# Performance work log

Measured on AMD Instinct MI355X. Metric: run time of the kernel, lower is better.

## Reference

```python
import jax, jax.numpy as jnp
import numpy as np

BN_EPS = 1e-3  # keras BatchNormalization default epsilon


def conv1x1(x, w):
    # x: [N,C,H,W], w: [O,C] (1x1 conv, no bias)
    return jnp.einsum('nchw,oc->nohw', x, w)


def bn(x, gamma, beta, mean, var):
    # inference-mode batchnorm over channel axis 1
    scale = gamma / jnp.sqrt(var + BN_EPS)
    shift = beta - mean * scale
    return x * scale[None, :, None, None] + shift[None, :, None, None]


def fourier_unit(x, w, gamma, beta, mean, var):
    # x: [N,C,H,W] NCHW. 1D rfft over W (matches tf.signal.rfft), normalized by sqrt(W).
    N, C, H, W = x.shape
    norm = jnp.sqrt(jnp.float32(W))
    f = jnp.fft.rfft(x / norm, axis=-1)          # [N,C,H,Wf] complex64, Wf=W//2+1
    Wf = f.shape[-1]
    # interleave re/im per channel: [N,C,2,H,Wf] -> [N,2C,H,Wf]
    ff = jnp.stack([jnp.real(f), jnp.imag(f)], axis=2).reshape(N, 2 * C, H, Wf)
    y = jax.nn.relu(bn(conv1x1(ff, w), gamma, beta, mean, var))  # [N,2C,H,Wf]
    Co = y.shape[1] // 2
    y = y.reshape(N, Co, 2, H, Wf)
    c = jax.lax.complex(y[:, :, 0], y[:, :, 1])
    return jnp.fft.irfft(c, n=W, axis=-1) * norm  # [N,Co,H,W]


def setup_inputs() -> dict:
    key = jax.random.key(0)
    ks = jax.random.split(key, 20)
    N, H, W, Cin = 8, 128, 128, 256
    fmaps = 256
    half = fmaps // 2  # 128

    def nrm(k, shape, s=0.05):
        return jax.random.normal(k, shape, dtype=jnp.float32) * s

    def bn_params(k, c):
        k1, k2, k3, k4 = jax.random.split(k, 4)
        gamma = jax.random.uniform(k1, (c,), dtype=jnp.float32) + 0.5
        beta = nrm(k2, (c,), 0.1)
        mean = nrm(k3, (c,), 0.1)
        var = jax.random.uniform(k4, (c,), dtype=jnp.float32) + 0.5
        return gamma, beta, mean, var

    x = jax.random.normal(ks[0], (N, H, W, Cin), dtype=jnp.float32)
    w1 = nrm(ks[1], (half, Cin))
    g1, b1, m1, v1 = bn_params(ks[2], half)
    fu_w = nrm(ks[3], (2 * half, 2 * half))
    fu_g, fu_b, fu_m, fu_v = bn_params(ks[4], 2 * half)
    lfu_w = nrm(ks[5], (2 * half, 2 * half))
    lfu_g, lfu_b, lfu_m, lfu_v = bn_params(ks[6], 2 * half)
    w2 = nrm(ks[7], (fmaps, half))
    return {
        'x': x, 'w1': w1, 'g1': g1, 'b1': b1, 'm1': m1, 'v1': v1,
        'fu_w': fu_w, 'fu_g': fu_g, 'fu_b': fu_b, 'fu_m': fu_m, 'fu_v': fu_v,
        'lfu_w': lfu_w, 'lfu_g': lfu_g, 'lfu_b': lfu_b, 'lfu_m': lfu_m, 'lfu_v': lfu_v,
        'w2': w2,
    }


def reference(x, w1, g1, b1, m1, v1,
              fu_w, fu_g, fu_b, fu_m, fu_v,
              lfu_w, lfu_g, lfu_b, lfu_m, lfu_v,
              w2):
    # NHWC -> NCHW (stride=1, no downsample)
    x = jnp.transpose(x, (0, 3, 1, 2))
    x = jax.nn.relu(bn(conv1x1(x, w1), g1, b1, m1, v1))  # [N,half,H,W]
    out = fourier_unit(x, fu_w, fu_g, fu_b, fu_m, fu_v)
    # local fourier unit: take first C//4 channels, fold 2x2 spatial patches into channels
    C = x.shape[1]
    xs = x[:, :C // 4]
    xs = jnp.concatenate(jnp.split(xs, 2, axis=2), axis=1)  # split H
    xs = jnp.concatenate(jnp.split(xs, 2, axis=3), axis=1)  # split W -> [N,C,H/2,W/2]
    xs = fourier_unit(xs, lfu_w, lfu_g, lfu_b, lfu_m, lfu_v)
    xs = jnp.tile(xs, (1, 1, 2, 2))  # back to [N,C,H,W]
    out = conv1x1(x + out + xs, w2)  # [N,fmaps,H,W]
    return jnp.transpose(out, (0, 2, 3, 1))  # NCHW -> NHWC
```

## Files before the change

kernel.cpp:

```cpp
#include <hip/hip_runtime.h>
#include <math.h>

typedef __attribute__((ext_vector_type(8))) short short8;
typedef __attribute__((ext_vector_type(4))) float f32x4;
typedef __attribute__((ext_vector_type(16))) float f32x16;

#define SW7b(r) (((r) & 7) << 4)
#define SW3b(r) (((r) & 3) << 4)
#define K15(r) (((r) & 15) << 4)
#define K7(r)  (((r) & 7) << 4)

static __device__ __forceinline__ unsigned short f2b(float f){
  unsigned u = __float_as_uint(f);
  u = (u + 0x7FFFu + ((u >> 16) & 1u)) >> 16;
  return (unsigned short)u;
}
static __device__ __forceinline__ float b2f(unsigned short u){
  return __uint_as_float(((unsigned)u) << 16);
}
static __device__ __forceinline__ unsigned pk2(float a, float b){
  unsigned r;
  asm("v_cvt_pk_bf16_f32 %0, %1, %2" : "=v"(r) : "v"(a), "v"(b));
  return r;
}
static __device__ __forceinline__ void gl16(const void* g, void* l) {
  __builtin_amdgcn_global_load_lds(
      (const __attribute__((address_space(1))) void*)g,
      (__attribute__((address_space(3))) void*)l, 16, 0, 0);
}

__global__ void k_wt(const float* __restrict__ w1, const float* __restrict__ fu_w,
                     const float* __restrict__ lfu_w, const float* __restrict__ w2,
                     const float* __restrict__ g1, const float* __restrict__ b1,
                     const float* __restrict__ m1, const float* __restrict__ v1,
                     const float* __restrict__ fg, const float* __restrict__ fb,
                     const float* __restrict__ fm, const float* __restrict__ fv,
                     const float* __restrict__ lg_, const float* __restrict__ lb_,
                     const float* __restrict__ lm_, const float* __restrict__ lv_,
                     unsigned short* __restrict__ w1b, unsigned short* __restrict__ fuwb,
                     unsigned short* __restrict__ lfuwb, unsigned short* __restrict__ w2b,
                     unsigned short* __restrict__ DFTf, unsigned short* __restrict__ IDFTf,
                     unsigned short* __restrict__ DFTl, unsigned short* __restrict__ IDFTl,
                     float* __restrict__ sc1, float* __restrict__ sh1,
                     float* __restrict__ scF, float* __restrict__ shF,
                     float* __restrict__ scL, float* __restrict__ shL) {
  int t = blockIdx.x * 256 + threadIdx.x;
  const float TPI = 6.283185307179586f;
  if (t < 32768) {
    { int co = t >> 8, k = t & 255; w1b[co * 256 + (k ^ ((co & 7) << 3))] = f2b(w1[t]); }
    { int co = t >> 7, k = t & 127; w2b[co * 128 + (k ^ ((co & 15) << 3))] = f2b(w2[t]); }
  }
  if (t < 65536) {
    int co = t >> 8, k = t & 255;
    fuwb[(size_t)(k >> 6) * 16384 + co * 64 + ((k & 63) ^ ((co & 7) << 3))] = f2b(fu_w[t]);
    lfuwb[co * 256 + (k ^ ((co & 7) << 3))] = f2b(lfu_w[t]);
  }
  if (t < 20480) {
    int m = t >> 7, w = t & 127; float v = 0.f;
    if (m < 130) {
      int wf = m >> 1; int ph = (wf * w) & 127;
      float ang = TPI * (float)ph / 128.f;
      v = ((m & 1) ? -sinf(ang) : cosf(ang)) * 0.08838834764831845f;
    }
    DFTf[m * 128 + (w ^ ((m & 15) << 3))] = f2b(v);
  }
  if (t < 24576) {
    int m = t / 192, k2 = t % 192; float v = 0.f;
    if (k2 < 130) {
      int wf = k2 >> 1; float a = (wf == 0 || wf == 64) ? 1.f : 2.f;
      int ph = (wf * m) & 127;
      float ang = TPI * (float)ph / 128.f;
      v = ((k2 & 1) ? -a * sinf(ang) : a * cosf(ang)) * 0.08838834764831845f;
    }
    IDFTf[m * 192 + (k2 ^ ((m & 7) << 3))] = f2b(v);
  }
  if (t < 5120) {
    int m = t >> 6, w = t & 63; float v = 0.f;
    if (m < 66) {
      int wf = m >> 1; int ph = (wf * w) & 63;
      float ang = TPI * (float)ph / 64.f;
      v = ((m & 1) ? -sinf(ang) : cosf(ang)) * 0.125f;
    }
    DFTl[m * 64 + (w ^ ((m & 7) << 3))] = f2b(v);
  }
  if (t < 6144) {
    int m = t / 96, k2 = t % 96; float v = 0.f;
    if (k2 < 66) {
      int wf = k2 >> 1; float a = (wf == 0 || wf == 32) ? 1.f : 2.f;
      int ph = (wf * m) & 63;
      float ang = TPI * (float)ph / 64.f;
      v = ((k2 & 1) ? -a * sinf(ang) : a * cosf(ang)) * 0.125f;
    }
    IDFTl[m * 96 + (k2 ^ ((m & 3) << 3))] = f2b(v);
  }
  if (t < 128) { float s = g1[t] * rsqrtf(v1[t] + 1e-3f); sc1[t] = s; sh1[t] = b1[t] - m1[t] * s; }
  if (t < 256) { float s = fg[t] * rsqrtf(fv[t] + 1e-3f); scF[t] = s; shF[t] = fb[t] - fm[t] * s; }
  if (t < 256) { float s = lg_[t] * rsqrtf(lv_[t] + 1e-3f); scL[t] = s; shL[t] = lb_[t] - lm_[t] * s; }
}

__global__ __launch_bounds__(512) void k_conv1(const unsigned short* __restrict__ A,
                                               const float* __restrict__ x,
                                               unsigned short* __restrict__ X1c,
                                               const float* __restrict__ scp,
                                               const float* __restrict__ shp) {
  __shared__ __align__(16) char A_s[128 * 512];
  __shared__ __align__(16) char B_s[2][32768];
  int t = threadIdx.x; int wid = t >> 6, l = t & 63;
  int wm = wid >> 2, wn = wid & 3;
  int m0 = wm * 64, n0 = wn * 64;
  int lr = l & 15, lg = l >> 4;
  size_t nh0 = (size_t)blockIdx.x * 2;
  const char* Ab = (const char*)A;
  const char* xrow = (const char*)(x + nh0 * 32768);
  #pragma unroll
  for (int i = 0; i < 8; i++) { int g = i * 512 + t; gl16(Ab + g * 16, A_s + g * 16); }
  #pragma unroll
  for (int i = 0; i < 4; i++) {
    int g = i * 512 + t; int w = g >> 3, o = g & 7;
    gl16(xrow + (size_t)w * 1024 + ((o * 16) ^ SW7b(w)), B_s[0] + g * 16);
  }
  f32x4 acc[4][4];
  #pragma unroll
  for (int mt = 0; mt < 4; mt++)
    #pragma unroll
    for (int nt = 0; nt < 4; nt++) acc[mt][nt] = (f32x4){0.f, 0.f, 0.f, 0.f};
  __syncthreads();
  for (int it = 0; it < 8; it++) {
    int kk = it * 32;
    if (it < 7) {
      #pragma unroll
      for (int i = 0; i < 4; i++) {
        int g = i * 512 + t; int w = g >> 3, o = g & 7;
        gl16(xrow + (size_t)w * 1024 + (kk + 32) * 4 + ((o * 16) ^ SW7b(w)),
             B_s[(it + 1) & 1] + g * 16);
      }
    }
    const char* Bc = B_s[it & 1];
    short8 af[4], bf[4];
    #pragma unroll
    for (int mt = 0; mt < 4; mt++) {
      int m = m0 + 16 * mt + lr;
      af[mt] = *(const short8*)(A_s + m * 512 + ((kk * 2 + lg * 16) ^ SW7b(m)));
    }
    #pragma unroll
    for (int nt = 0; nt < 4; nt++) {
      int w = n0 + 16 * nt + lr;
      float4 f0 = *(const float4*)(Bc + w * 128 + ((lg * 32) ^ SW7b(w)));
      float4 f1 = *(const float4*)(Bc + w * 128 + ((lg * 32 + 16) ^ SW7b(w)));
      short8 bb;
      bb[0] = (short)f2b(f0.x); bb[1] = (short)f2b(f0.y);
      bb[2] = (short)f2b(f0.z); bb[3] = (short)f2b(f0.w);
      bb[4] = (short)f2b(f1.x); bb[5] = (short)f2b(f1.y);
      bb[6] = (short)f2b(f1.z); bb[7] = (short)f2b(f1.w);
      bf[nt] = bb;
    }
    #pragma unroll
    for (int mt = 0; mt < 4; mt++)
      #pragma unroll
      for (int nt = 0; nt < 4; nt++)
        acc[mt][nt] = __builtin_amdgcn_mfma_f32_16x16x32_bf16(af[mt], bf[nt], acc[mt][nt], 0, 0, 0);
    __syncthreads();
  }
  #pragma unroll
  for (int nt = 0; nt < 4; nt++) {
    int wcol = n0 + 16 * nt + lr;
    char* xout = (char*)X1c + (nh0 + (wcol >> 7)) * 32768;
    int w = wcol & 127;
    #pragma unroll
    for (int mt = 0; mt < 4; mt++) {
      int rb = m0 + 16 * mt + lg * 4;
      float4 s4 = *(const float4*)&scp[rb];
      float4 h4 = *(const float4*)&shp[rb];
      f32x4 v = acc[mt][nt];
      *(unsigned short*)(xout + (rb + 0) * 256 + ((w * 2) ^ K15(rb + 0))) = f2b(fmaxf(v[0] * s4.x + h4.x, 0.f));
      *(unsigned short*)(xout + (rb + 1) * 256 + ((w * 2) ^ K15(rb + 1))) = f2b(fmaxf(v[1] * s4.y + h4.y, 0.f));
      *(unsigned short*)(xout + (rb + 2) * 256 + ((w * 2) ^ K15(rb + 2))) = f2b(fmaxf(v[2] * s4.z + h4.z, 0.f));
      *(unsigned short*)(xout + (rb + 3) * 256 + ((w * 2) ^ K15(rb + 3))) = f2b(fmaxf(v[3] * s4.w + h4.w, 0.f));
    }
  }
}

__global__ __launch_bounds__(256) void k_lfu(const unsigned short* __restrict__ DFTm,
                                             const unsigned short* __restrict__ lfuw,
                                             const unsigned short* __restrict__ IDFTm,
                                             const unsigned short* __restrict__ X1c,
                                             const float* __restrict__ scp,
                                             const float* __restrict__ shp,
                                             unsigned short* __restrict__ XSO) {
  __shared__ __align__(16) char SH[81920];
  char* M   = SH;
  char* S0  = SH + 16384;
  char* FFl = SH + 32768;
  char* Yl  = SH + 57344;
  int t = threadIdx.x, wid = t >> 6, l = t & 63, lr = l & 15, lg = l >> 4;
  int b = blockIdx.x; int n = b >> 6, h2 = b & 63;
  {
    #pragma unroll
    for (int i = 0; i < 3; i++) { int g = i * 256 + t; if (g < 640) gl16((const char*)DFTm + g * 16, M + g * 16); }
    #pragma unroll
    for (int i = 0; i < 4; i++) { int g = i * 256 + t; gl16((const char*)lfuw + g * 16, S0 + g * 16); }
    #pragma unroll
    for (int i = 0; i < 8; i++) {
      int u = i * 256 + t;
      if (u < 1920) *(unsigned*)(FFl + 33 * 512 + u * 4) = 0u;
    }
  }
  __syncthreads();
  {
    short8 bfp[2][2];
    #pragma unroll
    for (int nt = 0; nt < 2; nt++) {
      int c2 = wid * 32 + 16 * nt + lr;
      int c0 = c2 & 31, hb = (c2 >> 5) & 1, wbq = (c2 >> 6) & 1;
      int half = wbq ^ ((c0 >> 3) & 1);
      const char* base = (const char*)X1c +
          ((size_t)(n * 128 + hb * 64 + h2) * 128 + c0) * 256 + half * 128;
      #pragma unroll
      for (int ki = 0; ki < 2; ki++) {
        int kb = ki * 64 + lg * 16;
        bfp[nt][ki] = *(const short8*)(base + (kb ^ SW7b(c2)));
      }
    }
    f32x4 acc[5][2];
    #pragma unroll
    for (int mt = 0; mt < 5; mt++) { acc[mt][0] = (f32x4){0,0,0,0}; acc[mt][1] = (f32x4){0,0,0,0}; }
    #pragma unroll
    for (int ki = 0; ki < 2; ki++) {
      int kb = ki * 64 + lg * 16;
      #pragma unroll
      for (int mt = 0; mt < 5; mt++) {
        int m = 16 * mt + lr;
        short8 af = *(const short8*)(M + m * 128 + (kb ^ SW7b(m)));
        #pragma unroll
        for (int nt = 0; nt < 2; nt++)
          acc[mt][nt] = __builtin_amdgcn_mfma_f32_16x16x32_bf16(af, bfp[nt][ki], acc[mt][nt], 0, 0, 0);
      }
    }
    #pragma unroll
    for (int nt = 0; nt < 2; nt++) {
      int c2 = wid * 32 + 16 * nt + lr;
      #pragma unroll
      for (int mt = 0; mt < 5; mt++) {
        int rb = 16 * mt + lg * 4;
        int wf0 = rb >> 1;
        f32x4 v = acc[mt][nt];
        if (wf0 < 33) {
          unsigned pk = (unsigned)f2b(v[0]) | ((unsigned)f2b(v[1]) << 16);
          *(unsigned*)(FFl + wf0 * 512 + ((4 * c2) ^ SW7b(wf0))) = pk;
        }
        if (wf0 + 1 < 33) {
          unsigned pk = (unsigned)f2b(v[2]) | ((unsigned)f2b(v[3]) << 16);
          *(unsigned*)(FFl + (wf0 + 1) * 512 + ((4 * c2) ^ SW7b(wf0 + 1))) = pk;
        }
      }
    }
  }
  __syncthreads();
  int wm2 = wid >> 1, wn2 = wid & 1;
  for (int ch = 0; ch < 8; ch++) {
    char* Mc = (ch & 1) ? M : S0;
    char* Mn = (ch & 1) ? S0 : M;
    if (ch < 7) {
      #pragma unroll
      for (int i = 0; i < 4; i++) {
        int g = i * 256 + t;
        gl16((const char*)lfuw + (size_t)(ch + 1) * 16384 + g * 16, Mn + g * 16);
      }
    } else {
      #pragma unroll
      for (int i = 0; i < 3; i++) {
        int g = i * 256 + t;
        if (g < 768) gl16((const char*)IDFTm + g * 16, Mn + g * 16);
      }
    }
    int NT = wn2 ? 1 : 2;
    f32x4 acc[2];
    acc[0] = (f32x4){0,0,0,0}; acc[1] = (f32x4){0,0,0,0};
    int lm = wm2 * 16 + lr;
    for (int kk = 0; kk < 256; kk += 32) {
      int kb = kk * 2 + lg * 16;
      short8 af = *(const short8*)(Mc + lm * 512 + (kb ^ SW7b(lm)));
      #pragma unroll
      for (int j = 0; j < 2; j++) {
        if (j < NT) {
          int wf = wn2 * 32 + 16 * j + lr;
          short8 bf = *(const short8*)(FFl + wf * 512 + (kb ^ SW7b(wf)));
          acc[j] = __builtin_amdgcn_mfma_f32_16x16x32_bf16(af, bf, acc[j], 0, 0, 0);
        }
      }
    }
    int co = ch * 32 + wm2 * 16 + lg * 4;
    float4 s4 = *(const float4*)&scp[co];
    float4 h4 = *(const float4*)&shp[co];
    int cc0 = co >> 1;
    #pragma unroll
    for (int j = 0; j < 2; j++) {
      if (j < NT) {
        int wf = wn2 * 32 + 16 * j + lr;
        f32x4 v = acc[j];
        float v0 = fmaxf(v[0] * s4.x + h4.x, 0.f);
        float v1 = fmaxf(v[1] * s4.y + h4.y, 0.f);
        float v2 = fmaxf(v[2] * s4.z + h4.z, 0.f);
        float v3 = fmaxf(v[3] * s4.w + h4.w, 0.f);
        unsigned p0 = (unsigned)f2b(v0) | ((unsigned)f2b(v1) << 16);
        unsigned p1 = (unsigned)f2b(v2) | ((unsigned)f2b(v3) << 16);
        *(unsigned*)(Yl + (cc0 + 0) * 192 + ((4 * wf) ^ SW3b(cc0 + 0))) = p0;
        *(unsigned*)(Yl + (cc0 + 1) * 192 + ((4 * wf) ^ SW3b(cc0 + 1))) = p1;
      }
    }
    __syncthreads();
  }
  {
    f32x4 acc[8];
    #pragma unroll
    for (int nt = 0; nt < 8; nt++) acc[nt] = (f32x4){0,0,0,0};
    int w = wid * 16 + lr;
    for (int kk = 0; kk < 96; kk += 32) {
      int kb = kk * 2 + lg * 16;
      short8 af = *(const short8*)(S0 + w * 192 + (kb ^ SW3b(w)));
      #pragma unroll
      for (int nt = 0; nt < 8; nt++) {
        int cc = 16 * nt + lr;
        short8 bf = *(const short8*)(Yl + cc * 192 + (kb ^ SW3b(cc)));
        acc[nt] = __builtin_amdgcn_mfma_f32_16x16x32_bf16(af, bf, acc[nt], 0, 0, 0);
      }
    }
    int w0 = wid * 16 + lg * 4;
    #pragma unroll
    for (int nt = 0; nt < 8; nt++) {
      int cc = 16 * nt + lr;
      f32x4 v = acc[nt];
      ushort4 o;
      o.x = f2b(v[0]); o.y = f2b(v[1]); o.z = f2b(v[2]); o.w = f2b(v[3]);
      *(ushort4*)(XSO + (((size_t)n * 128 + cc) * 64 + h2) * 64 + w0) = o;
    }
  }
}

__global__ __launch_bounds__(1024, 4) void k_fu(const unsigned short* __restrict__ DFTm,
                                                const unsigned short* __restrict__ fuw,
                                                const unsigned short* __restrict__ IDFTm,
                                                const unsigned short* __restrict__ w2m,
                                                const unsigned short* __restrict__ X1c,
                                                const unsigned short* __restrict__ XSO,
                                                const float* __restrict__ scF,
                                                const float* __restrict__ shF,
                                                float* __restrict__ out) {
  __shared__ __align__(16) char SH[161792];
  char* R0 = SH;
  char* R1 = SH + 40960;
  char* R2 = SH + 73728;
  char* R3 = SH + 122880;
  int t = threadIdx.x, wid = t >> 6, l = t & 63;
  int lc = l & 31, hf = l >> 5;
  size_t nh = blockIdx.x;
  int n = (int)(nh >> 7), hh = (int)(nh & 127);
  const char* xb = (const char*)X1c + nh * 32768;

  #pragma unroll
  for (int i = 0; i < 3; i++) {
    int g = i * 1024 + t;
    if (g < 2560) gl16((const char*)DFTm + (size_t)g * 16, R0 + g * 16);
  }
  *(unsigned*)(R2 + 80 * 512 + t * 8) = 0u;
  *(unsigned*)(R2 + 80 * 512 + t * 8 + 4) = 0u;
  __syncthreads();
  {
    #pragma unroll
    for (int i = 0; i < 2; i++) {
      int g = i * 1024 + t;
      gl16((const char*)fuw + (size_t)g * 16, R1 + g * 16);
    }
    int mb = wid & 3, nb = wid >> 2;
    int c = nb * 32 + lc;
    short8 bfp[8];
    #pragma unroll
    for (int ks = 0; ks < 8; ks++)
      bfp[ks] = *(const short8*)(xb + (size_t)c * 256 + ((ks * 32 + hf * 16) ^ K15(c)));
    f32x16 acc0 = {0}, acc1 = {0};
    bool x2 = (wid < 4);
    int c2b = wid * 32 + lc;
    #pragma unroll
    for (int ks = 0; ks < 8; ks++) {
      int ko = ks * 32 + hf * 16;
      int m = mb * 32 + lc;
      short8 af = *(const short8*)(R0 + (size_t)m * 256 + (ko ^ K15(m)));
      acc0 = __builtin_amdgcn_mfma_f32_32x32x16_bf16(af, bfp[ks], acc0, 0, 0, 0);
      if (x2) {
        int m2 = 128 + lc;
        short8 af2 = *(const short8*)(R0 + (size_t)m2 * 256 + (ko ^ K15(m2)));
        short8 bf2 = *(const short8*)(xb + (size_t)c2b * 256 + (ko ^ K15(c2b)));
        acc1 = __builtin_amdgcn_mfma_f32_32x32x16_bf16(af2, bf2, acc1, 0, 0, 0);
      }
    }
    #pragma unroll
    for (int q = 0; q < 4; q++) {
      int wfe = mb * 16 + 4 * q + 2 * hf;
      unsigned p0 = pk2(acc0[4 * q + 0], acc0[4 * q + 1]);
      unsigned p1 = pk2(acc0[4 * q + 2], acc0[4 * q + 3]);
      *(unsigned*)(R2 + (size_t)wfe * 512 + ((4 * c) ^ K15(wfe))) = p0;
      *(unsigned*)(R2 + (size_t)(wfe + 1) * 512 + ((4 * c) ^ K15(wfe + 1))) = p1;
    }
    if (x2) {
      #pragma unroll
      for (int q = 0; q < 4; q++) {
        int wfe = 64 + 4 * q + 2 * hf;
        unsigned p0 = pk2(acc1[4 * q + 0], acc1[4 * q + 1]);
        unsigned p1 = pk2(acc1[4 * q + 2], acc1[4 * q + 3]);
        *(unsigned*)(R2 + (size_t)wfe * 512 + ((4 * c2b) ^ K15(wfe))) = p0;
        *(unsigned*)(R2 + (size_t)(wfe + 1) * 512 + ((4 * c2b) ^ K15(wfe + 1))) = p1;
      }
    }
  }
  {
    int mb = wid >> 1, odd = wid & 1;
    int co = mb * 32 + lc;
    f32x16 pa = {0}, pb = {0};
    int wfA = (odd ? 32 : 0) + lc;
    int wfB = 64 + lc;
    #pragma unroll
    for (int ch = 0; ch < 4; ch++) {
      char* Mc = (ch & 1) ? R0 : R1;
      char* Mn = (ch & 1) ? R1 : R0;
      __syncthreads();
      if (ch < 3) {
        #pragma unroll
        for (int i = 0; i < 2; i++) {
          int g = i * 1024 + t;
          gl16((const char*)fuw + (size_t)(ch + 1) * 32768 + (size_t)g * 16, Mn + g * 16);
        }
      } else {
        #pragma unroll
        for (int i = 0; i < 2; i++) {
          int g = i * 1024 + t;
          gl16((const char*)w2m + (size_t)g * 16, Mn + g * 16);
        }
      }
      #pragma unroll
      for (int ks = 0; ks < 4; ks++) {
        int ko = ks * 32 + hf * 16;
        short8 af = *(const short8*)(Mc + (size_t)co * 128 + (ko ^ K7(co)));
        int kg = (ch * 4 + ks) * 32 + hf * 16;
        short8 bfA = *(const short8*)(R2 + (size_t)wfA * 512 + (kg ^ K15(wfA)));
        pa = __builtin_amdgcn_mfma_f32_32x32x16_bf16(af, bfA, pa, 0, 0, 0);
        if (!odd) {
          short8 bfB = *(const short8*)(R2 + (size_t)wfB * 512 + (kg ^ K15(wfB)));
          pb = __builtin_amdgcn_mfma_f32_32x32x16_bf16(af, bfB, pb, 0, 0, 0);
        }
      }
    }
    #pragma unroll
    for (int q = 0; q < 4; q++) {
      int co0 = mb * 32 + 8 * q + 4 * hf;
      float4 s4 = *(const float4*)&scF[co0];
      float4 h4 = *(const float4*)&shF[co0];
      int cc0 = co0 >> 1;
      {
        float v0 = fmaxf(pa[4 * q + 0] * s4.x + h4.x, 0.f);
        float v1 = fmaxf(pa[4 * q + 1] * s4.y + h4.y, 0.f);
        float v2 = fmaxf(pa[4 * q + 2] * s4.z + h4.z, 0.f);
        float v3 = fmaxf(pa[4 * q + 3] * s4.w + h4.w, 0.f);
        *(unsigned*)(R3 + (size_t)(cc0 + 0) * 304 + 4 * wfA) = pk2(v0, v1);
        *(unsigned*)(R3 + (size_t)(cc0 + 1) * 304 + 4 * wfA) = pk2(v2, v3);
      }
      if (!odd && lc < 12) {
        float v0 = fmaxf(pb[4 * q + 0] * s4.x + h4.x, 0.f);
        float v1 = fmaxf(pb[4 * q + 1] * s4.y + h4.y, 0.f);
        float v2 = fmaxf(pb[4 * q + 2] * s4.z + h4.z, 0.f);
        float v3 = fmaxf(pb[4 * q + 3] * s4.w + h4.w, 0.f);
        *(unsigned*)(R3 + (size_t)(cc0 + 0) * 304 + 4 * wfB) = pk2(v0, v1);
        *(unsigned*)(R3 + (size_t)(cc0 + 1) * 304 + 4 * wfB) = pk2(v2, v3);
      }
    }
  }
  __syncthreads();
  #pragma unroll
  for (int i = 0; i < 3; i++) {
    int g = i * 1024 + t;
    gl16((const char*)IDFTm + (size_t)g * 16, R2 + g * 16);
  }
  #pragma unroll
  for (int i = 0; i < 2; i++) {
    int g = i * 1024 + t;
    gl16((const char*)w2m + 32768 + (size_t)g * 16, R0 + g * 16);
  }
  __syncthreads();
  {
    int mb = wid & 3, nb = wid >> 2;
    int mw = mb * 32 + lc;
    int cc = nb * 32 + lc;
    ushort4 rx[4], rs[4];
    #pragma unroll
    for (int q = 0; q < 4; q++) {
      int w0 = mb * 32 + 8 * q + 4 * hf;
      rx[q] = *(const ushort4*)(xb + (size_t)cc * 256 + ((2 * w0) ^ K15(cc)));
      rs[q] = *(const ushort4*)(XSO + (((size_t)n * 128 + cc) * 64 + (hh & 63)) * 64 + (w0 & 63));
    }
    f32x16 p3 = {0};
    #pragma unroll
    for (int ks = 0; ks < 9; ks++) {
      int ko = ks * 32 + hf * 16;
      short8 af = *(const short8*)(R2 + (size_t)mw * 384 + (ko ^ K7(mw)));
      short8 bf = *(const short8*)(R3 + (size_t)cc * 304 + ko);
      p3 = __builtin_amdgcn_mfma_f32_32x32x16_bf16(af, bf, p3, 0, 0, 0);
    }
    __syncthreads();
    #pragma unroll
    for (int q = 0; q < 4; q++) {
      int w0 = mb * 32 + 8 * q + 4 * hf;
      float f0 = p3[4 * q + 0] + b2f(rx[q].x) + b2f(rs[q].x);
      float f1 = p3[4 * q + 1] + b2f(rx[q].y) + b2f(rs[q].y);
      float f2_ = p3[4 * q + 2] + b2f(rx[q].z) + b2f(rs[q].z);
      float f3 = p3[4 * q + 3] + b2f(rx[q].w) + b2f(rs[q].w);
      *(unsigned short*)(R3 + (size_t)(w0 + 0) * 256 + ((2 * cc) ^ K15(w0 + 0))) = f2b(f0);
      *(unsigned short*)(R3 + (size_t)(w0 + 1) * 256 + ((2 * cc) ^ K15(w0 + 1))) = f2b(f1);
      *(unsigned short*)(R3 + (size_t)(w0 + 2) * 256 + ((2 * cc) ^ K15(w0 + 2))) = f2b(f2_);
      *(unsigned short*)(R3 + (size_t)(w0 + 3) * 256 + ((2 * cc) ^ K15(w0 + 3))) = f2b(f3);
    }
  }
  __syncthreads();
  {
    int mb = wid & 3, nb = wid >> 2;
    int mw = mb * 32 + lc;
    int rco = nb * 32 + lc;
    #pragma unroll
    for (int ck = 0; ck < 2; ck++) {
      const char* Mc = ck ? R0 : R1;
      f32x16 p4 = {0};
      #pragma unroll
      for (int ks = 0; ks < 8; ks++) {
        int ko = ks * 32 + hf * 16;
        short8 af = *(const short8*)(R3 + (size_t)mw * 256 + (ko ^ K15(mw)));
        short8 bf = *(const short8*)(Mc + (size_t)rco * 256 + (ko ^ K15(rco)));
        p4 = __builtin_amdgcn_mfma_f32_32x32x16_bf16(af, bf, p4, 0, 0, 0);
      }
      float* obase = out + (nh * 128 + mb * 32) * 256 + ck * 128 + nb * 32 + lc;
      #pragma unroll
      for (int q = 0; q < 4; q++) {
        #pragma unroll
        for (int i = 0; i < 4; i++) {
          int wrow = 8 * q + 4 * hf + i;
          obase[(size_t)wrow * 256] = p4[4 * q + i];
        }
      }
    }
  }
}

extern "C" void kernel_launch(void* const* d_in, const int* in_sizes, int n_in,
                              void* d_out, int out_size, void* d_ws, size_t ws_size,
                              hipStream_t stream) {
  const float* x     = (const float*)d_in[0];
  const float* w1    = (const float*)d_in[1];
  const float* g1    = (const float*)d_in[2];
  const float* b1    = (const float*)d_in[3];
  const float* m1    = (const float*)d_in[4];
  const float* v1    = (const float*)d_in[5];
  const float* fu_w  = (const float*)d_in[6];
  const float* fu_g  = (const float*)d_in[7];
  const float* fu_b  = (const float*)d_in[8];
  const float* fu_m  = (const float*)d_in[9];
  const float* fu_v  = (const float*)d_in[10];
  const float* lfu_w = (const float*)d_in[11];
  const float* lfu_g = (const float*)d_in[12];
  const float* lfu_b = (const float*)d_in[13];
  const float* lfu_m = (const float*)d_in[14];
  const float* lfu_v = (const float*)d_in[15];
  const float* w2    = (const float*)d_in[16];
  float* out = (float*)d_out;

  char* p = (char*)d_ws;
  unsigned short* X1c = (unsigned short*)p; p += 33554432;
  unsigned short* XSO = (unsigned short*)p; p += 8388608;
  unsigned short* w1b   = (unsigned short*)p; p += 65536;
  unsigned short* fuwb  = (unsigned short*)p; p += 131072;
  unsigned short* lfuwb = (unsigned short*)p; p += 131072;
  unsigned short* w2b   = (unsigned short*)p; p += 65536;
  unsigned short* DFTf  = (unsigned short*)p; p += 40960;
  unsigned short* IDFTf = (unsigned short*)p; p += 49152;
  unsigned short* DFTl  = (unsigned short*)p; p += 10240;
  unsigned short* IDFTl = (unsigned short*)p; p += 12288;
  float* sc1 = (float*)p; p += 512;
  float* sh1 = (float*)p; p += 512;
  float* scF = (float*)p; p += 1024;
  float* shF = (float*)p; p += 1024;
  float* scL = (float*)p; p += 1024;
  float* shL = (float*)p; p += 1024;

  k_wt<<<dim3(256), dim3(256), 0, stream>>>(w1, fu_w, lfu_w, w2, g1, b1, m1, v1,
                                            fu_g, fu_b, fu_m, fu_v, lfu_g, lfu_b, lfu_m, lfu_v,
                                            w1b, fuwb, lfuwb, w2b, DFTf, IDFTf, DFTl, IDFTl,
                                            sc1, sh1, scF, shF, scL, shL);
  k_conv1<<<dim3(512), dim3(512), 0, stream>>>(w1b, x, X1c, sc1, sh1);
  k_lfu<<<dim3(512), dim3(256), 0, stream>>>(DFTl, lfuwb, IDFTl, X1c, scL, shL, XSO);
  k_fu<<<dim3(1024), dim3(1024), 0, stream>>>(DFTf, fuwb, IDFTf, w2b, X1c, XSO, scF, shF, out);
}
```

Baseline: 137.6 us.

## Read FU weights and DFT matrices from global memory instead of LDS staging

```diff
diff --git a/kernel.cpp b/kernel.cpp
--- a/kernel.cpp
+++ b/kernel.cpp
@@ -8,7 +8,6 @@
 #define SW7b(r) (((r) & 7) << 4)
 #define SW3b(r) (((r) & 3) << 4)
 #define K15(r) (((r) & 15) << 4)
-#define K7(r)  (((r) & 7) << 4)
 
 static __device__ __forceinline__ unsigned short f2b(float f){
   unsigned u = __float_as_uint(f);
@@ -48,11 +47,11 @@
   const float TPI = 6.283185307179586f;
   if (t < 32768) {
     { int co = t >> 8, k = t & 255; w1b[co * 256 + (k ^ ((co & 7) << 3))] = f2b(w1[t]); }
-    { int co = t >> 7, k = t & 127; w2b[co * 128 + (k ^ ((co & 15) << 3))] = f2b(w2[t]); }
+    w2b[t] = f2b(w2[t]);
   }
   if (t < 65536) {
     int co = t >> 8, k = t & 255;
-    fuwb[(size_t)(k >> 6) * 16384 + co * 64 + ((k & 63) ^ ((co & 7) << 3))] = f2b(fu_w[t]);
+    fuwb[t] = f2b(fu_w[t]);
     lfuwb[co * 256 + (k ^ ((co & 7) << 3))] = f2b(lfu_w[t]);
   }
   if (t < 20480) {
@@ -62,7 +61,7 @@
       float ang = TPI * (float)ph / 128.f;
       v = ((m & 1) ? -sinf(ang) : cosf(ang)) * 0.08838834764831845f;
     }
-    DFTf[m * 128 + (w ^ ((m & 15) << 3))] = f2b(v);
+    DFTf[t] = f2b(v);
   }
   if (t < 24576) {
     int m = t / 192, k2 = t % 192; float v = 0.f;
@@ -72,7 +71,7 @@
       float ang = TPI * (float)ph / 128.f;
       v = ((k2 & 1) ? -a * sinf(ang) : a * cosf(ang)) * 0.08838834764831845f;
     }
-    IDFTf[m * 192 + (k2 ^ ((m & 7) << 3))] = f2b(v);
+    IDFTf[m * 192 + k2] = f2b(v);
   }
   if (t < 5120) {
     int m = t >> 6, w = t & 63; float v = 0.f;
@@ -337,7 +336,7 @@
   }
 }
 
-__global__ __launch_bounds__(1024, 4) void k_fu(const unsigned short* __restrict__ DFTm,
+__global__ __launch_bounds__(1024, 2) void k_fu(const unsigned short* __restrict__ DFTm,
                                                 const unsigned short* __restrict__ fuw,
                                                 const unsigned short* __restrict__ IDFTm,
                                                 const unsigned short* __restrict__ w2m,
@@ -346,31 +345,16 @@
                                                 const float* __restrict__ scF,
                                                 const float* __restrict__ shF,
                                                 float* __restrict__ out) {
-  __shared__ __align__(16) char SH[161792];
-  char* R0 = SH;
-  char* R1 = SH + 40960;
-  char* R2 = SH + 73728;
-  char* R3 = SH + 122880;
+  __shared__ __align__(16) char SH[79872];
+  char* FF = SH;
+  char* Yb = SH + 40960;
   int t = threadIdx.x, wid = t >> 6, l = t & 63;
   int lc = l & 31, hf = l >> 5;
   size_t nh = blockIdx.x;
   int n = (int)(nh >> 7), hh = (int)(nh & 127);
   const char* xb = (const char*)X1c + nh * 32768;
 
-  #pragma unroll
-  for (int i = 0; i < 3; i++) {
-    int g = i * 1024 + t;
-    if (g < 2560) gl16((const char*)DFTm + (size_t)g * 16, R0 + g * 16);
-  }
-  *(unsigned*)(R2 + 80 * 512 + t * 8) = 0u;
-  *(unsigned*)(R2 + 80 * 512 + t * 8 + 4) = 0u;
-  __syncthreads();
-  {
-    #pragma unroll
-    for (int i = 0; i < 2; i++) {
-      int g = i * 1024 + t;
-      gl16((const char*)fuw + (size_t)g * 16, R1 + g * 16);
-    }
+  {
     int mb = wid & 3, nb = wid >> 2;
     int c = nb * 32 + lc;
     short8 bfp[8];
@@ -382,14 +366,14 @@
     int c2b = wid * 32 + lc;
     #pragma unroll
     for (int ks = 0; ks < 8; ks++) {
-      int ko = ks * 32 + hf * 16;
+      int koe = ks * 16 + hf * 8;
       int m = mb * 32 + lc;
-      short8 af = *(const short8*)(R0 + (size_t)m * 256 + (ko ^ K15(m)));
+      short8 af = *(const short8*)(DFTm + (size_t)m * 128 + koe);
       acc0 = __builtin_amdgcn_mfma_f32_32x32x16_bf16(af, bfp[ks], acc0, 0, 0, 0);
       if (x2) {
         int m2 = 128 + lc;
-        short8 af2 = *(const short8*)(R0 + (size_t)m2 * 256 + (ko ^ K15(m2)));
-        short8 bf2 = *(const short8*)(xb + (size_t)c2b * 256 + (ko ^ K15(c2b)));
+        short8 af2 = *(const short8*)(DFTm + (size_t)m2 * 128 + koe);
+        short8 bf2 = *(const short8*)(xb + (size_t)c2b * 256 + ((ks * 32 + hf * 16) ^ K15(c2b)));
         acc1 = __builtin_amdgcn_mfma_f32_32x32x16_bf16(af2, bf2, acc1, 0, 0, 0);
       }
     }
@@ -398,8 +382,8 @@
       int wfe = mb * 16 + 4 * q + 2 * hf;
       unsigned p0 = pk2(acc0[4 * q + 0], acc0[4 * q + 1]);
       unsigned p1 = pk2(acc0[4 * q + 2], acc0[4 * q + 3]);
-      *(unsigned*)(R2 + (size_t)wfe * 512 + ((4 * c) ^ K15(wfe))) = p0;
-      *(unsigned*)(R2 + (size_t)(wfe + 1) * 512 + ((4 * c) ^ K15(wfe + 1))) = p1;
+      *(unsigned*)(FF + (size_t)wfe * 512 + ((4 * c) ^ K15(wfe))) = p0;
+      *(unsigned*)(FF + (size_t)(wfe + 1) * 512 + ((4 * c) ^ K15(wfe + 1))) = p1;
     }
     if (x2) {
       #pragma unroll
@@ -407,11 +391,12 @@
         int wfe = 64 + 4 * q + 2 * hf;
         unsigned p0 = pk2(acc1[4 * q + 0], acc1[4 * q + 1]);
         unsigned p1 = pk2(acc1[4 * q + 2], acc1[4 * q + 3]);
-        *(unsigned*)(R2 + (size_t)wfe * 512 + ((4 * c2b) ^ K15(wfe))) = p0;
-        *(unsigned*)(R2 + (size_t)(wfe + 1) * 512 + ((4 * c2b) ^ K15(wfe + 1))) = p1;
-      }
-    }
-  }
+        *(unsigned*)(FF + (size_t)wfe * 512 + ((4 * c2b) ^ K15(wfe))) = p0;
+        *(unsigned*)(FF + (size_t)(wfe + 1) * 512 + ((4 * c2b) ^ K15(wfe + 1))) = p1;
+      }
+    }
+  }
+  __syncthreads();
   {
     int mb = wid >> 1, odd = wid & 1;
     int co = mb * 32 + lc;
@@ -419,34 +404,15 @@
     int wfA = (odd ? 32 : 0) + lc;
     int wfB = 64 + lc;
     #pragma unroll
-    for (int ch = 0; ch < 4; ch++) {
-      char* Mc = (ch & 1) ? R0 : R1;
-      char* Mn = (ch & 1) ? R1 : R0;
-      __syncthreads();
-      if (ch < 3) {
-        #pragma unroll
-        for (int i = 0; i < 2; i++) {
-          int g = i * 1024 + t;
-          gl16((const char*)fuw + (size_t)(ch + 1) * 32768 + (size_t)g * 16, Mn + g * 16);
-        }
-      } else {
-        #pragma unroll
-        for (int i = 0; i < 2; i++) {
-          int g = i * 1024 + t;
-          gl16((const char*)w2m + (size_t)g * 16, Mn + g * 16);
-        }
-      }
-      #pragma unroll
-      for (int ks = 0; ks < 4; ks++) {
-        int ko = ks * 32 + hf * 16;
-        short8 af = *(const short8*)(Mc + (size_t)co * 128 + (ko ^ K7(co)));
-        int kg = (ch * 4 + ks) * 32 + hf * 16;
-        short8 bfA = *(const short8*)(R2 + (size_t)wfA * 512 + (kg ^ K15(wfA)));
-        pa = __builtin_amdgcn_mfma_f32_32x32x16_bf16(af, bfA, pa, 0, 0, 0);
-        if (!odd) {
-          short8 bfB = *(const short8*)(R2 + (size_t)wfB * 512 + (kg ^ K15(wfB)));
-          pb = __builtin_amdgcn_mfma_f32_32x32x16_bf16(af, bfB, pb, 0, 0, 0);
-        }
+    for (int ks = 0; ks < 16; ks++) {
+      int koe = ks * 16 + hf * 8;
+      short8 af = *(const short8*)(fuw + (size_t)co * 256 + koe);
+      int kg = ks * 32 + hf * 16;
+      short8 bfA = *(const short8*)(FF + (size_t)wfA * 512 + (kg ^ K15(wfA)));
+      pa = __builtin_amdgcn_mfma_f32_32x32x16_bf16(af, bfA, pa, 0, 0, 0);
+      if (!odd) {
+        short8 bfB = *(const short8*)(FF + (size_t)wfB * 512 + (kg ^ K15(wfB)));
+        pb = __builtin_amdgcn_mfma_f32_32x32x16_bf16(af, bfB, pb, 0, 0, 0);
       }
     }
     #pragma unroll
@@ -460,29 +426,18 @@
         float v1 = fmaxf(pa[4 * q + 1] * s4.y + h4.y, 0.f);
         float v2 = fmaxf(pa[4 * q + 2] * s4.z + h4.z, 0.f);
         float v3 = fmaxf(pa[4 * q + 3] * s4.w + h4.w, 0.f);
-        *(unsigned*)(R3 + (size_t)(cc0 + 0) * 304 + 4 * wfA) = pk2(v0, v1);
-        *(unsigned*)(R3 + (size_t)(cc0 + 1) * 304 + 4 * wfA) = pk2(v2, v3);
+        *(unsigned*)(Yb + (size_t)(cc0 + 0) * 304 + 4 * wfA) = pk2(v0, v1);
+        *(unsigned*)(Yb + (size_t)(cc0 + 1) * 304 + 4 * wfA) = pk2(v2, v3);
       }
       if (!odd && lc < 12) {
         float v0 = fmaxf(pb[4 * q + 0] * s4.x + h4.x, 0.f);
         float v1 = fmaxf(pb[4 * q + 1] * s4.y + h4.y, 0.f);
         float v2 = fmaxf(pb[4 * q + 2] * s4.z + h4.z, 0.f);
         float v3 = fmaxf(pb[4 * q + 3] * s4.w + h4.w, 0.f);
-        *(unsigned*)(R3 + (size_t)(cc0 + 0) * 304 + 4 * wfB) = pk2(v0, v1);
-        *(unsigned*)(R3 + (size_t)(cc0 + 1) * 304 + 4 * wfB) = pk2(v2, v3);
-      }
-    }
-  }
-  __syncthreads();
-  #pragma unroll
-  for (int i = 0; i < 3; i++) {
-    int g = i * 1024 + t;
-    gl16((const char*)IDFTm + (size_t)g * 16, R2 + g * 16);
-  }
-  #pragma unroll
-  for (int i = 0; i < 2; i++) {
-    int g = i * 1024 + t;
-    gl16((const char*)w2m + 32768 + (size_t)g * 16, R0 + g * 16);
+        *(unsigned*)(Yb + (size_t)(cc0 + 0) * 304 + 4 * wfB) = pk2(v0, v1);
+        *(unsigned*)(Yb + (size_t)(cc0 + 1) * 304 + 4 * wfB) = pk2(v2, v3);
+      }
+    }
   }
   __syncthreads();
   {
@@ -499,12 +454,11 @@
     f32x16 p3 = {0};
     #pragma unroll
     for (int ks = 0; ks < 9; ks++) {
-      int ko = ks * 32 + hf * 16;
-      short8 af = *(const short8*)(R2 + (size_t)mw * 384 + (ko ^ K7(mw)));
-      short8 bf = *(const short8*)(R3 + (size_t)cc * 304 + ko);
+      int koe = ks * 16 + hf * 8;
+      short8 af = *(const short8*)(IDFTm + (size_t)mw * 192 + koe);
+      short8 bf = *(const short8*)(Yb + (size_t)cc * 304 + ks * 32 + hf * 16);
       p3 = __builtin_amdgcn_mfma_f32_32x32x16_bf16(af, bf, p3, 0, 0, 0);
     }
-    __syncthreads();
     #pragma unroll
     for (int q = 0; q < 4; q++) {
       int w0 = mb * 32 + 8 * q + 4 * hf;
@@ -512,10 +466,10 @@
       float f1 = p3[4 * q + 1] + b2f(rx[q].y) + b2f(rs[q].y);
       float f2_ = p3[4 * q + 2] + b2f(rx[q].z) + b2f(rs[q].z);
       float f3 = p3[4 * q + 3] + b2f(rx[q].w) + b2f(rs[q].w);
-      *(unsigned short*)(R3 + (size_t)(w0 + 0) * 256 + ((2 * cc) ^ K15(w0 + 0))) = f2b(f0);
-      *(unsigned short*)(R3 + (size_t)(w0 + 1) * 256 + ((2 * cc) ^ K15(w0 + 1))) = f2b(f1);
-      *(unsigned short*)(R3 + (size_t)(w0 + 2) * 256 + ((2 * cc) ^ K15(w0 + 2))) = f2b(f2_);
-      *(unsigned short*)(R3 + (size_t)(w0 + 3) * 256 + ((2 * cc) ^ K15(w0 + 3))) = f2b(f3);
+      *(unsigned short*)(FF + (size_t)(w0 + 0) * 256 + ((2 * cc) ^ K15(w0 + 0))) = f2b(f0);
+      *(unsigned short*)(FF + (size_t)(w0 + 1) * 256 + ((2 * cc) ^ K15(w0 + 1))) = f2b(f1);
+      *(unsigned short*)(FF + (size_t)(w0 + 2) * 256 + ((2 * cc) ^ K15(w0 + 2))) = f2b(f2_);
+      *(unsigned short*)(FF + (size_t)(w0 + 3) * 256 + ((2 * cc) ^ K15(w0 + 3))) = f2b(f3);
     }
   }
   __syncthreads();
@@ -525,13 +479,12 @@
     int rco = nb * 32 + lc;
     #pragma unroll
     for (int ck = 0; ck < 2; ck++) {
-      const char* Mc = ck ? R0 : R1;
       f32x16 p4 = {0};
       #pragma unroll
       for (int ks = 0; ks < 8; ks++) {
-        int ko = ks * 32 + hf * 16;
-        short8 af = *(const short8*)(R3 + (size_t)mw * 256 + (ko ^ K15(mw)));
-        short8 bf = *(const short8*)(Mc + (size_t)rco * 256 + (ko ^ K15(rco)));
+        int koe = ks * 16 + hf * 8;
+        short8 af = *(const short8*)(FF + (size_t)mw * 256 + ((ks * 32 + hf * 16) ^ K15(mw)));
+        short8 bf = *(const short8*)(w2m + (size_t)(ck * 128 + rco) * 128 + koe);
         p4 = __builtin_amdgcn_mfma_f32_32x32x16_bf16(af, bf, p4, 0, 0, 0);
       }
       float* obase = out + (nh * 128 + mb * 32) * 256 + ck * 128 + nb * 32 + lc;
```

Result: slower. 196.4 us (+42.7%).
